# Optimization experiments

Measured on AMD Instinct MI355X. Metric: run time of the kernel, lower is better.

Reference implementation:

```python
import math
import jax, jax.numpy as jnp
import numpy as np

N_HEADS = 16
THETA = 10000.0


def _rope_cos_sin(S, head_dim):
    half = head_dim // 2
    inv_freq = 1.0 / (THETA ** (jnp.arange(half, dtype=jnp.float32) / half))
    t = jnp.arange(S, dtype=jnp.float32)
    freqs = t[:, None] * inv_freq[None, :]  # [S, half]
    return jnp.cos(freqs), jnp.sin(freqs)


def _apply_rope(x, cos, sin):
    # x: [B, H, S, D] float32; cos/sin: [S, D//2]
    half = x.shape[-1] // 2
    x1, x2 = x[..., :half], x[..., half:]
    c = cos[None, None, :, :]
    s = sin[None, None, :, :]
    return jnp.concatenate([x1 * c - x2 * s, x1 * s + x2 * c], axis=-1)


def setup_inputs() -> dict:
    key = jax.random.key(0)
    k1, k2, k3 = jax.random.split(key, 3)
    B, S, D = 4, 2048, 1024
    x = jax.random.normal(k1, (B, S, D), dtype=jnp.float32)
    w_qkv = jax.random.normal(k2, (3 * D, D), dtype=jnp.float32) * (1.0 / math.sqrt(D))
    w_out = jax.random.normal(k3, (D, D), dtype=jnp.float32) * (1.0 / math.sqrt(D))
    return {"x": x, "w_qkv": w_qkv, "w_out": w_out}


def reference(x, w_qkv, w_out):
    B, S, D = x.shape
    H = N_HEADS
    hd = D // H

    qkv = x @ w_qkv.T  # [B, S, 3D]
    q, k, v = jnp.split(qkv, 3, axis=-1)

    def reshape(t):
        return t.reshape(B, S, H, hd).transpose(0, 2, 1, 3)  # [B,H,S,hd]

    q, k, v = reshape(q), reshape(k), reshape(v)

    cos, sin = _rope_cos_sin(S, hd)
    q = _apply_rope(q.astype(jnp.float32), cos, sin).astype(x.dtype)
    k = _apply_rope(k.astype(jnp.float32), cos, sin).astype(x.dtype)

    scale = math.sqrt(hd)
    scores = jnp.einsum("bhsd,bhtd->bhst", q, k) / scale  # [B,H,S,S]
    causal = jnp.tril(jnp.ones((S, S), dtype=bool))
    scores = jnp.where(causal[None, None], scores, -jnp.inf)
    attn = jax.nn.softmax(scores.astype(jnp.float32), axis=-1).astype(x.dtype)

    out = jnp.einsum("bhst,bhtd->bhsd", attn, v)  # [B,H,S,hd]
    out = out.transpose(0, 2, 1, 3).reshape(B, S, D)
    return out @ w_out.T
```

## Files before the change

kernel.cpp:

```cpp
#include <hip/hip_runtime.h>
#include <hip/hip_bf16.h>

#define DEV static __device__ __forceinline__

typedef unsigned short u16;
typedef unsigned int u32;
typedef __attribute__((ext_vector_type(8))) short short8;
typedef __attribute__((ext_vector_type(4))) float f32x4;
typedef __attribute__((ext_vector_type(16))) float f32x16;
typedef __attribute__((ext_vector_type(4))) u32 u32x4;

static constexpr int Bsz = 4, Ssz = 2048, Dsz = 1024, Hn = 16, HD = 64;
static constexpr int Mrows = Bsz * Ssz;

DEV u16 f2bu(float f) {
  union { float f; u32 u; } a; a.f = f;
  u32 u = a.u;
  u32 r = (u + 0x7FFFu + ((u >> 16) & 1u)) >> 16;
  return (u16)r;
}
DEV float b2f(u16 v) {
  union { u32 u; float f; } a; a.u = ((u32)v) << 16;
  return a.f;
}
DEV u32 pk2(float lo, float hi2) {
  __hip_bfloat162 t = __float22bfloat162_rn(make_float2(lo, hi2));
  u32 r; __builtin_memcpy(&r, &t, 4); return r;
}
DEV f32x16 mfma3232(short8 a, short8 b, f32x16 c) {
  return __builtin_amdgcn_mfma_f32_32x32x16_bf16(a, b, c, 0, 0, 0);
}
DEV float max3f(float a, float b, float c) { return fmaxf(fmaxf(a, b), c); }
DEV float ex2(float x) { return __builtin_amdgcn_exp2f(x); }

__global__ void k_cast(const float4* __restrict__ in, ushort4* __restrict__ out, int n4) {
  int stride = gridDim.x * blockDim.x;
  for (int i = blockIdx.x * blockDim.x + threadIdx.x; i < n4; i += stride) {
    float4 v = in[i];
    ushort4 o;
    o.x = f2bu(v.x); o.y = f2bu(v.y); o.z = f2bu(v.z); o.w = f2bu(v.w);
    out[i] = o;
  }
}

__global__ void k_ropetab(float2* __restrict__ cst) {
  int i = blockIdx.x * blockDim.x + threadIdx.x;
  if (i >= Ssz * 32) return;
  int s = i >> 5, d = i & 31;
  float inv = powf(10000.0f, -(float)d / 32.0f);
  float fr = (float)s * inv;
  cst[i] = make_float2(cosf(fr), sinf(fr));
}

__global__ __launch_bounds__(256) void k_vtrans(const u16* __restrict__ qkv,
                                                u16* __restrict__ vt) {
  __shared__ u16 tile[64][68];
  const int t = threadIdx.x;
  const int bh = blockIdx.y;
  const int b = bh >> 4, h = bh & 15;
  const int s0 = blockIdx.x * 64;
#pragma unroll
  for (int it = 0; it < 4; ++it) {
    int idx = it * 256 + t;
    int d4 = (idx & 15) * 4;
    int sl = idx >> 4;
    ushort4 v = *(const ushort4*)(qkv + ((size_t)(b * Ssz + s0 + sl)) * 3072 + 2048 + h * 64 + d4);
    *(ushort4*)&tile[sl][d4] = v;
  }
  __syncthreads();
#pragma unroll
  for (int it = 0; it < 4; ++it) {
    int idx = it * 256 + t;
    int sl4 = (idx & 15) * 4;
    int d = idx >> 4;
    ushort4 o;
    o.x = tile[sl4 + 0][d];
    o.y = tile[sl4 + 1][d];
    o.z = tile[sl4 + 2][d];
    o.w = tile[sl4 + 3][d];
    *(ushort4*)(vt + ((size_t)(bh * 64 + d)) * Ssz + s0 + sl4) = o;
  }
}

DEV void cp16(const u16* g, u16* l) {
  __builtin_amdgcn_global_load_lds((const __attribute__((address_space(1))) u32*)g,
                                   (__attribute__((address_space(3))) u32*)l, 16, 0, 0);
}

template <bool OUTBF16>
__global__ __launch_bounds__(256, 2) void k_gemm(const u16* __restrict__ A,
                                                 const u16* __restrict__ W,
                                                 void* __restrict__ C, int N, int K,
                                                 const float2* __restrict__ cst, int cpx) {
  __shared__ __align__(16) u16 Asm[2][128 * 64];
  __shared__ __align__(16) u16 Bsm[2][128 * 64];
  const int tid = threadIdx.x;
  const int wid = tid >> 6, lane = tid & 63;
  const int lr = lane & 15, u = lane >> 4;
  const int wm = wid >> 1, wn = wid & 1;

  const int wg = blockIdx.x;
  const int xcd = wg & 7;
  const int j = wg >> 3;
  const int brow = (j / cpx) * 128;
  const int bcol = (xcd * cpx + j % cpx) * 128;

  const int rw = wid * 32 + (lane >> 3);
  const int octS = ((lane & 7) ^ (rw & 7)) * 8;
  const u16* aS = A + (size_t)(brow + rw) * K + octS;
  const u16* bS = W + (size_t)(bcol + rw) * K + octS;
  const int dBase = wid * 2048 + lane * 8;

  const int aBase = (wm * 64 + lr) * 64;
  const int bBase = (wn * 64 + lr) * 64;
  const int o0 = (u ^ (lane & 7)) * 8;
  const int o1 = ((4 + u) ^ (lane & 7)) * 8;

  f32x4 acc[4][4];
#pragma unroll
  for (int i = 0; i < 4; ++i)
#pragma unroll
    for (int j2 = 0; j2 < 4; ++j2) acc[i][j2] = (f32x4){0.f, 0.f, 0.f, 0.f};

  const int nt = K >> 6;

#define STG(kk, bb)                                          \
  do {                                                       \
    cp16(aS + (kk), Asm[bb] + dBase);                        \
    cp16(aS + (size_t)8 * K + (kk), Asm[bb] + dBase + 512);  \
    cp16(aS + (size_t)16 * K + (kk), Asm[bb] + dBase + 1024);\
    cp16(aS + (size_t)24 * K + (kk), Asm[bb] + dBase + 1536);\
    cp16(bS + (kk), Bsm[bb] + dBase);                        \
    cp16(bS + (size_t)8 * K + (kk), Bsm[bb] + dBase + 512);  \
    cp16(bS + (size_t)16 * K + (kk), Bsm[bb] + dBase + 1024);\
    cp16(bS + (size_t)24 * K + (kk), Bsm[bb] + dBase + 1536);\
  } while (0)

  STG(0, 0);

  for (int t = 0; t < nt; ++t) {
    asm volatile("s_waitcnt vmcnt(0)" ::: "memory");
    __builtin_amdgcn_s_barrier();
    if (t + 1 < nt) STG((t + 1) << 6, (t + 1) & 1);
    const u16* ab = Asm[t & 1];
    const u16* bb = Bsm[t & 1];
    short8 a0[4], a1[4], b0[4], b1[4];
#pragma unroll
    for (int mr = 0; mr < 4; ++mr) {
      a0[mr] = *(const short8*)(ab + aBase + mr * 1024 + o0);
      a1[mr] = *(const short8*)(ab + aBase + mr * 1024 + o1);
    }
#pragma unroll
    for (int nr = 0; nr < 4; ++nr) {
      b0[nr] = *(const short8*)(bb + bBase + nr * 1024 + o0);
      b1[nr] = *(const short8*)(bb + bBase + nr * 1024 + o1);
    }
    __builtin_amdgcn_s_setprio(1);
#pragma unroll
    for (int mr = 0; mr < 4; ++mr)
#pragma unroll
      for (int nr = 0; nr < 4; ++nr)
        acc[mr][nr] =
            __builtin_amdgcn_mfma_f32_16x16x32_bf16(a0[mr], b0[nr], acc[mr][nr], 0, 0, 0);
#pragma unroll
    for (int mr = 0; mr < 4; ++mr)
#pragma unroll
      for (int nr = 0; nr < 4; ++nr)
        acc[mr][nr] =
            __builtin_amdgcn_mfma_f32_16x16x32_bf16(a1[mr], b1[nr], acc[mr][nr], 0, 0, 0);
    __builtin_amdgcn_s_setprio(0);
  }
#undef STG

  const int row0 = brow + wm * 64 + u * 4;
  const int col0 = bcol + wn * 64 + lr;
  if (OUTBF16) {
    const int rmode = (bcol < 1024) ? 0 : (bcol < 2048) ? 1 : 2;
    const float sc = (rmode == 0) ? 0.18033688f : 1.0f;
#pragma unroll
    for (int mr = 0; mr < 4; ++mr)
#pragma unroll
      for (int r = 0; r < 4; ++r) {
        const int row = row0 + mr * 16 + r;
        size_t base = (size_t)row * N + col0;
        u16* cp = (u16*)C + base;
        if (rmode < 2) {
          const int s = row & 2047;
          const float2 c0 = cst[s * 32 + lr];
          const float2 c1 = cst[s * 32 + 16 + lr];
          const float x10 = acc[mr][0][r], x11 = acc[mr][1][r];
          const float x20 = acc[mr][2][r], x21 = acc[mr][3][r];
          cp[0]  = f2bu((x10 * c0.x - x20 * c0.y) * sc);
          cp[16] = f2bu((x11 * c1.x - x21 * c1.y) * sc);
          cp[32] = f2bu((x10 * c0.y + x20 * c0.x) * sc);
          cp[48] = f2bu((x11 * c1.y + x21 * c1.x) * sc);
        } else {
#pragma unroll
          for (int nr = 0; nr < 4; ++nr) cp[nr * 16] = f2bu(acc[mr][nr][r]);
        }
      }
  } else {
#pragma unroll
    for (int mr = 0; mr < 4; ++mr)
#pragma unroll
      for (int r = 0; r < 4; ++r) {
        size_t base = (size_t)(row0 + mr * 16 + r) * N + col0;
#pragma unroll
        for (int nr = 0; nr < 4; ++nr) ((float*)C)[base + nr * 16] = acc[mr][nr][r];
      }
  }
}

__global__ __launch_bounds__(256, 4) void k_attn(const u16* __restrict__ qkv,
                                                 const u16* __restrict__ vt,
                                                 u16* __restrict__ obuf) {
  __shared__ __align__(16) u16 Ksm[2][64 * 64];
  __shared__ __align__(16) u16 Vsm[2][64 * 64];

  const int tid = threadIdx.x;
  const int wid = tid >> 6;
  const int lane = tid & 63;
  const int l31 = lane & 31;
  const int hi = lane >> 5;
  const int r7 = l31 & 7;

  const int fid = blockIdx.x;
  const int a = fid & 3, bq = (fid >> 8) & 3;
  const int bh = (fid >> 2) & 63;
  const int sel = a ^ bq;
  const int qt = (sel == 0) ? bq : (sel == 1) ? 7 - bq : (sel == 2) ? 8 + bq : 15 - bq;

  const int b = bh >> 4;
  const int h = bh & 15;

  const float NEG = -__builtin_inff();

  const int srow = lane >> 3;
  const int scol = ((lane & 7) ^ srow) * 8;
  const u16* ksrc0 = qkv + (size_t)(b * Ssz + wid * 16 + srow) * 3072 + 1024 + h * 64 + scol;
  const u16* ksrc1 = ksrc0 + (size_t)8 * 3072;
  const u16* vsrc0 = vt + ((size_t)bh * 64 + wid * 16 + srow) * Ssz + scol;
  const u16* vsrc1 = vsrc0 + (size_t)8 * Ssz;
  u16* kD0 = Ksm[0] + wid * 1024;
  u16* vD0 = Vsm[0] + wid * 1024;

  const int q0 = qt * 128;
  const int qrow = q0 + (wid << 5) + l31;

  const u16* qptr = qkv + (size_t)(b * Ssz + qrow) * 3072 + h * 64 + hi * 8;
  short8 qf[4];
#pragma unroll
  for (int s = 0; s < 4; ++s) qf[s] = *(const short8*)(qptr + s * 16);

  f32x16 o0 = {0.f}, o1 = {0.f};
  float m = NEG, lsum = 0.f;

  const int ntiles = 2 * qt + 2;
  const int lastT = 2 * qt + (wid >> 1);

  cp16(ksrc0, kD0);
  cp16(ksrc1, kD0 + 512);
  cp16(vsrc0, vD0);
  cp16(vsrc1, vD0 + 512);

  const u16* kS0 = ksrc0 + (size_t)64 * 3072;
  const u16* kS1 = ksrc1 + (size_t)64 * 3072;
  const u16* vS0 = vsrc0 + 64;
  const u16* vS1 = vsrc1 + 64;

  for (int t = 0; t < ntiles; ++t) {
    __syncthreads();
    if (t + 1 < ntiles) {
      const int nb = (t + 1) & 1;
      cp16(kS0, kD0 + nb * 4096);
      cp16(kS1, kD0 + nb * 4096 + 512);
      cp16(vS0, vD0 + nb * 4096);
      cp16(vS1, vD0 + nb * 4096 + 512);
      kS0 += (size_t)64 * 3072;
      kS1 += (size_t)64 * 3072;
      vS0 += 64;
      vS1 += 64;
    }
    if (t > lastT) continue;

    const u16* kbuf = Ksm[t & 1];
    const u16* vbuf = Vsm[t & 1];
    const int kv0 = t << 6;

    f32x16 st0 = {0.f}, st1 = {0.f};
    __builtin_amdgcn_s_setprio(1);
#pragma unroll
    for (int s = 0; s < 4; ++s) {
      const int slot = (((2 * s + hi) ^ r7) << 3);
      short8 k0 = *(const short8*)(kbuf + l31 * 64 + slot);
      short8 k1 = *(const short8*)(kbuf + (32 + l31) * 64 + slot);
      st0 = mfma3232(k0, qf[s], st0);
      st1 = mfma3232(k1, qf[s], st1);
    }
    __builtin_amdgcn_s_setprio(0);

    if (t == lastT) {
      const int kb0 = kv0 + 4 * hi;
#pragma unroll
      for (int r = 0; r < 16; ++r) {
        const int ko = (r & 3) + 8 * (r >> 2);
        if (kb0 + ko > qrow) st0[r] = NEG;
        if (kb0 + 32 + ko > qrow) st1[r] = NEG;
      }
    }

    float c0 = max3f(st0[0], st0[1], st0[2]);
    c0 = max3f(c0, st0[3], st1[0]);
    c0 = max3f(c0, st1[1], st1[2]);
    c0 = fmaxf(c0, st1[3]);
    float c1 = max3f(st0[4], st0[5], st0[6]);
    c1 = max3f(c1, st0[7], st1[4]);
    c1 = max3f(c1, st1[5], st1[6]);
    c1 = fmaxf(c1, st1[7]);
    float c2 = max3f(st0[8], st0[9], st0[10]);
    c2 = max3f(c2, st0[11], st1[8]);
    c2 = max3f(c2, st1[9], st1[10]);
    c2 = fmaxf(c2, st1[11]);
    float c3 = max3f(st0[12], st0[13], st0[14]);
    c3 = max3f(c3, st0[15], st1[12]);
    c3 = max3f(c3, st1[13], st1[14]);
    c3 = fmaxf(c3, st1[15]);
    float pm = fmaxf(max3f(c0, c1, c2), c3);
    pm = fmaxf(pm, __shfl_xor(pm, 32));

    if (!__all(pm <= m + 8.0f)) {
      const float mn = fmaxf(m, pm);
      const float corr = ex2(m - mn);
      lsum *= corr;
      o0 *= corr;
      o1 *= corr;
      m = mn;
    }

    float rsp[4] = {0.f, 0.f, 0.f, 0.f};
#pragma unroll
    for (int r = 0; r < 16; ++r) {
      const float p0 = ex2(st0[r] - m);
      const float p1 = ex2(st1[r] - m);
      st0[r] = p0;
      st1[r] = p1;
      rsp[r & 3] += p0 + p1;
    }
    float rs = (rsp[0] + rsp[1]) + (rsp[2] + rsp[3]);
    rs += __shfl_xor(rs, 32);
    lsum += rs;

    u32 wa[8], wb[8];
#pragma unroll
    for (int g = 0; g < 4; ++g) {
      wa[g] = pk2(st0[4 * g + 0], st0[4 * g + 1]);
      wb[g] = pk2(st0[4 * g + 2], st0[4 * g + 3]);
      wa[4 + g] = pk2(st1[4 * g + 0], st1[4 * g + 1]);
      wb[4 + g] = pk2(st1[4 * g + 2], st1[4 * g + 3]);
    }

#pragma unroll
    for (int s = 0; s < 4; ++s) {
      const u32 uA0 = wa[2 * s], uA1 = wa[2 * s + 1];
      const u32 uB0 = wb[2 * s], uB1 = wb[2 * s + 1];
      const u32 tA0 = __shfl_xor(uA0, 32), tA1 = __shfl_xor(uA1, 32);
      const u32 tB0 = __shfl_xor(uB0, 32), tB1 = __shfl_xor(uB1, 32);
      u32x4 pw;
      pw.x = hi ? tA1 : uA0;
      pw.y = hi ? tB1 : uB0;
      pw.z = hi ? uA1 : tA0;
      pw.w = hi ? uB1 : tB0;
      short8 pfrag = *(short8*)&pw;
      const int slot = (((2 * s + hi) ^ r7) << 3);
      short8 v0 = *(const short8*)(vbuf + l31 * 64 + slot);
      short8 v1 = *(const short8*)(vbuf + (32 + l31) * 64 + slot);
      __builtin_amdgcn_s_setprio(1);
      o0 = mfma3232(v0, pfrag, o0);
      o1 = mfma3232(v1, pfrag, o1);
      __builtin_amdgcn_s_setprio(0);
    }
  }

  const float inv = 1.0f / lsum;
  u16* orow = obuf + (size_t)(b * Ssz + qrow) * 1024 + h * 64;
#pragma unroll
  for (int j = 0; j < 4; ++j) {
    ushort4 s0, s1;
    s0.x = f2bu(o0[4 * j + 0] * inv);
    s0.y = f2bu(o0[4 * j + 1] * inv);
    s0.z = f2bu(o0[4 * j + 2] * inv);
    s0.w = f2bu(o0[4 * j + 3] * inv);
    s1.x = f2bu(o1[4 * j + 0] * inv);
    s1.y = f2bu(o1[4 * j + 1] * inv);
    s1.z = f2bu(o1[4 * j + 2] * inv);
    s1.w = f2bu(o1[4 * j + 3] * inv);
    *(ushort4*)(orow + 8 * j + 4 * hi) = s0;
    *(ushort4*)(orow + 32 + 8 * j + 4 * hi) = s1;
  }
}

extern "C" void kernel_launch(void* const* d_in, const int* in_sizes, int n_in,
                              void* d_out, int out_size, void* d_ws, size_t ws_size,
                              hipStream_t stream) {
  const float* x = (const float*)d_in[0];
  const float* wqkv = (const float*)d_in[1];
  const float* wout = (const float*)d_in[2];

  char* ws = (char*)d_ws;
  u16* xb      = (u16*)(ws + 0);
  u16* wqkvb   = (u16*)(ws + 16777216);
  u16* woutb   = (u16*)(ws + 23068672);
  u16* qkv     = (u16*)(ws + 25165824);
  u16* vt      = (u16*)(ws + 75497472);
  u16* obuf    = (u16*)(ws + 92274688);
  float2* cst  = (float2*)(ws + 109051904);

  k_cast<<<2048, 256, 0, stream>>>((const float4*)x, (ushort4*)xb, Mrows * Dsz / 4);
  k_cast<<<2048, 256, 0, stream>>>((const float4*)wqkv, (ushort4*)wqkvb, 3 * Dsz * Dsz / 4);
  k_cast<<<1024, 256, 0, stream>>>((const float4*)wout, (ushort4*)woutb, Dsz * Dsz / 4);
  k_ropetab<<<256, 256, 0, stream>>>(cst);

  k_gemm<true><<<1536, 256, 0, stream>>>(xb, wqkvb, qkv, 3072, 1024, cst, 3);

  k_vtrans<<<dim3(32, 64), 256, 0, stream>>>(qkv, vt);

  k_attn<<<1024, 256, 0, stream>>>(qkv, vt, obuf);

  k_gemm<false><<<512, 256, 0, stream>>>(obuf, woutb, d_out, 1024, 1024, nullptr, 1);
}
```

Measured before the change: 190.2 us.

## Fuse V transpose into QKV GEMM epilogue via LDS-staged coalesced stores

Removes the separate V-transpose kernel. The QKV GEMM epilogue now writes the V tile transposed straight into the vt buffer. The Q/K output (after RoPE) and the V output are both staged through LDS so global stores become 16-byte coalesced writes instead of scattered 2-byte stores. This removes one launch and an extra read/write pass over V, at the cost of an extra LDS round trip and barriers in the epilogue. V is no longer written into the qkv buffer, so attention must read V only from vt.

```diff
diff --git a/kernel.cpp b/kernel.cpp
--- a/kernel.cpp
+++ b/kernel.cpp
@@ -52,36 +52,6 @@
   cst[i] = make_float2(cosf(fr), sinf(fr));
 }
 
-__global__ __launch_bounds__(256) void k_vtrans(const u16* __restrict__ qkv,
-                                                u16* __restrict__ vt) {
-  __shared__ u16 tile[64][68];
-  const int t = threadIdx.x;
-  const int bh = blockIdx.y;
-  const int b = bh >> 4, h = bh & 15;
-  const int s0 = blockIdx.x * 64;
-#pragma unroll
-  for (int it = 0; it < 4; ++it) {
-    int idx = it * 256 + t;
-    int d4 = (idx & 15) * 4;
-    int sl = idx >> 4;
-    ushort4 v = *(const ushort4*)(qkv + ((size_t)(b * Ssz + s0 + sl)) * 3072 + 2048 + h * 64 + d4);
-    *(ushort4*)&tile[sl][d4] = v;
-  }
-  __syncthreads();
-#pragma unroll
-  for (int it = 0; it < 4; ++it) {
-    int idx = it * 256 + t;
-    int sl4 = (idx & 15) * 4;
-    int d = idx >> 4;
-    ushort4 o;
-    o.x = tile[sl4 + 0][d];
-    o.y = tile[sl4 + 1][d];
-    o.z = tile[sl4 + 2][d];
-    o.w = tile[sl4 + 3][d];
-    *(ushort4*)(vt + ((size_t)(bh * 64 + d)) * Ssz + s0 + sl4) = o;
-  }
-}
-
 DEV void cp16(const u16* g, u16* l) {
   __builtin_amdgcn_global_load_lds((const __attribute__((address_space(1))) u32*)g,
                                    (__attribute__((address_space(3))) u32*)l, 16, 0, 0);
@@ -91,9 +61,9 @@
 __global__ __launch_bounds__(256, 2) void k_gemm(const u16* __restrict__ A,
                                                  const u16* __restrict__ W,
                                                  void* __restrict__ C, int N, int K,
-                                                 const float2* __restrict__ cst, int cpx) {
-  __shared__ __align__(16) u16 Asm[2][128 * 64];
-  __shared__ __align__(16) u16 Bsm[2][128 * 64];
+                                                 const float2* __restrict__ cst, int cpx,
+                                                 u16* __restrict__ vtp) {
+  __shared__ __align__(16) u16 SMEM[32768];
   const int tid = threadIdx.x;
   const int wid = tid >> 6, lane = tid & 63;
   const int lr = lane & 15, u = lane >> 4;
@@ -124,16 +94,18 @@
 
   const int nt = K >> 6;
 
-#define STG(kk, bb)                                          \
-  do {                                                       \
-    cp16(aS + (kk), Asm[bb] + dBase);                        \
-    cp16(aS + (size_t)8 * K + (kk), Asm[bb] + dBase + 512);  \
-    cp16(aS + (size_t)16 * K + (kk), Asm[bb] + dBase + 1024);\
-    cp16(aS + (size_t)24 * K + (kk), Asm[bb] + dBase + 1536);\
-    cp16(bS + (kk), Bsm[bb] + dBase);                        \
-    cp16(bS + (size_t)8 * K + (kk), Bsm[bb] + dBase + 512);  \
-    cp16(bS + (size_t)16 * K + (kk), Bsm[bb] + dBase + 1024);\
-    cp16(bS + (size_t)24 * K + (kk), Bsm[bb] + dBase + 1536);\
+#define STG(kk, bb)                                                    \
+  do {                                                                 \
+    u16* ad = SMEM + (bb)*8192 + dBase;                                \
+    u16* bd = SMEM + 16384 + (bb)*8192 + dBase;                        \
+    cp16(aS + (kk), ad);                                               \
+    cp16(aS + (size_t)8 * K + (kk), ad + 512);                         \
+    cp16(aS + (size_t)16 * K + (kk), ad + 1024);                       \
+    cp16(aS + (size_t)24 * K + (kk), ad + 1536);                       \
+    cp16(bS + (kk), bd);                                               \
+    cp16(bS + (size_t)8 * K + (kk), bd + 512);                         \
+    cp16(bS + (size_t)16 * K + (kk), bd + 1024);                       \
+    cp16(bS + (size_t)24 * K + (kk), bd + 1536);                       \
   } while (0)
 
   STG(0, 0);
@@ -142,8 +114,8 @@
     asm volatile("s_waitcnt vmcnt(0)" ::: "memory");
     __builtin_amdgcn_s_barrier();
     if (t + 1 < nt) STG((t + 1) << 6, (t + 1) & 1);
-    const u16* ab = Asm[t & 1];
-    const u16* bb = Bsm[t & 1];
+    const u16* ab = SMEM + (t & 1) * 8192;
+    const u16* bb = SMEM + 16384 + (t & 1) * 8192;
     short8 a0[4], a1[4], b0[4], b1[4];
 #pragma unroll
     for (int mr = 0; mr < 4; ++mr) {
@@ -172,34 +144,62 @@
   }
 #undef STG
 
-  const int row0 = brow + wm * 64 + u * 4;
-  const int col0 = bcol + wn * 64 + lr;
   if (OUTBF16) {
+    __syncthreads();
     const int rmode = (bcol < 1024) ? 0 : (bcol < 2048) ? 1 : 2;
-    const float sc = (rmode == 0) ? 0.18033688f : 1.0f;
-#pragma unroll
-    for (int mr = 0; mr < 4; ++mr)
-#pragma unroll
-      for (int r = 0; r < 4; ++r) {
-        const int row = row0 + mr * 16 + r;
-        size_t base = (size_t)row * N + col0;
-        u16* cp = (u16*)C + base;
-        if (rmode < 2) {
-          const int s = row & 2047;
+    if (rmode < 2) {
+      const float sc = (rmode == 0) ? 0.18033688f : 1.0f;
+#pragma unroll
+      for (int mr = 0; mr < 4; ++mr)
+#pragma unroll
+        for (int r = 0; r < 4; ++r) {
+          const int row = wm * 64 + mr * 16 + u * 4 + r;
+          const int s = (brow + row) & 2047;
           const float2 c0 = cst[s * 32 + lr];
           const float2 c1 = cst[s * 32 + 16 + lr];
           const float x10 = acc[mr][0][r], x11 = acc[mr][1][r];
           const float x20 = acc[mr][2][r], x21 = acc[mr][3][r];
-          cp[0]  = f2bu((x10 * c0.x - x20 * c0.y) * sc);
-          cp[16] = f2bu((x11 * c1.x - x21 * c1.y) * sc);
-          cp[32] = f2bu((x10 * c0.y + x20 * c0.x) * sc);
-          cp[48] = f2bu((x11 * c1.y + x21 * c1.x) * sc);
-        } else {
-#pragma unroll
-          for (int nr = 0; nr < 4; ++nr) cp[nr * 16] = f2bu(acc[mr][nr][r]);
+          u16* lp = SMEM + row * 136 + wn * 64 + lr;
+          lp[0]  = f2bu((x10 * c0.x - x20 * c0.y) * sc);
+          lp[16] = f2bu((x11 * c1.x - x21 * c1.y) * sc);
+          lp[32] = f2bu((x10 * c0.y + x20 * c0.x) * sc);
+          lp[48] = f2bu((x11 * c1.y + x21 * c1.x) * sc);
         }
+      __syncthreads();
+      u16* cp = (u16*)C;
+#pragma unroll
+      for (int i = 0; i < 8; ++i) {
+        const int e = i * 2048 + tid * 8;
+        const int row = e >> 7, col = e & 127;
+        short8 v = *(const short8*)(SMEM + row * 136 + col);
+        *(short8*)(cp + (size_t)(brow + row) * N + bcol + col) = v;
       }
+    } else {
+#pragma unroll
+      for (int mr = 0; mr < 4; ++mr)
+#pragma unroll
+        for (int nr = 0; nr < 4; ++nr)
+#pragma unroll
+          for (int r = 0; r < 4; ++r) {
+            const int dl = wn * 64 + nr * 16 + lr;
+            const int sl = wm * 64 + mr * 16 + u * 4 + r;
+            SMEM[dl * 136 + sl] = f2bu(acc[mr][nr][r]);
+          }
+      __syncthreads();
+      const int bb2 = brow >> 11;
+      const int sbase = brow & 2047;
+#pragma unroll
+      for (int i = 0; i < 8; ++i) {
+        const int e = i * 2048 + tid * 8;
+        const int dl = e >> 7, sl = e & 127;
+        const int gd = (bcol - 2048) + dl;
+        short8 v = *(const short8*)(SMEM + dl * 136 + sl);
+        *(short8*)(vtp + (size_t)(bb2 * 1024 + gd) * 2048 + sbase + sl) = v;
+      }
+    }
   } else {
+    const int row0 = brow + wm * 64 + u * 4;
+    const int col0 = bcol + wn * 64 + lr;
 #pragma unroll
     for (int mr = 0; mr < 4; ++mr)
 #pragma unroll
@@ -420,11 +420,9 @@
   k_cast<<<1024, 256, 0, stream>>>((const float4*)wout, (ushort4*)woutb, Dsz * Dsz / 4);
   k_ropetab<<<256, 256, 0, stream>>>(cst);
 
-  k_gemm<true><<<1536, 256, 0, stream>>>(xb, wqkvb, qkv, 3072, 1024, cst, 3);
-
-  k_vtrans<<<dim3(32, 64), 256, 0, stream>>>(qkv, vt);
+  k_gemm<true><<<1536, 256, 0, stream>>>(xb, wqkvb, qkv, 3072, 1024, cst, 3, vt);
 
   k_attn<<<1024, 256, 0, stream>>>(qkv, vt, obuf);
 
-  k_gemm<false><<<512, 256, 0, stream>>>(obuf, woutb, d_out, 1024, 1024, nullptr, 1);
-}
+  k_gemm<false><<<512, 256, 0, stream>>>(obuf, woutb, d_out, 1024, 1024, nullptr, 1, nullptr);
+}
```

Result: faster. 179.3 us (-5.8%).
